# Kernel tuning notes

Measured on AMD Instinct MI355X. Metric: run time of the kernel, lower is better.

Reference implementation:

```python
import jax, jax.numpy as jnp
import numpy as np

N = 100000   # num nodes
D = 128      # node_emb_dim
R = 8        # num_relations
E = 1600000  # num edges


def setup_inputs() -> dict:
    key = jax.random.key(0)
    k0, k1, k2, k3, k4 = jax.random.split(key, 5)
    x = jax.random.normal(k0, (N, D), dtype=jnp.float32)
    edge_index = jax.random.randint(k1, (2, E), 0, N, dtype=jnp.int32)
    edge_type = jax.random.randint(k2, (E,), 0, R, dtype=jnp.int32)
    scale = 1.0 / np.sqrt(D)
    W = (jax.random.normal(k3, (R, D, D), dtype=jnp.float32) * scale)       # per-relation weight
    W_root = (jax.random.normal(k4, (D, D), dtype=jnp.float32) * scale)     # root (self-loop) weight
    bias = jnp.zeros((D,), dtype=jnp.float32)
    return {"x": x, "W": W, "W_root": W_root, "bias": bias,
            "edge_index": edge_index, "edge_type": edge_type}


def reference(x, W, W_root, bias, edge_index, edge_type):
    # PyG RGCNConv (num_bases=None, aggr='mean', root_weight=True, bias=True):
    # out_i = x_i @ W_root + bias + sum_r mean_{j in N_r(i)} x_j @ W_r
    # Mean aggregation is linear, so aggregate neighbor features per (node, relation)
    # first, then apply the per-relation transform (avoids [E,D,D] intermediates).
    src, dst = edge_index[0], edge_index[1]
    seg = dst * R + edge_type                                   # [E] segment id per (dst, rel)
    cnt = jax.ops.segment_sum(jnp.ones((E,), x.dtype), seg, num_segments=N * R)  # [N*R]
    sums = jax.ops.segment_sum(x[src], seg, num_segments=N * R)                   # [N*R, D]
    mean = sums / jnp.maximum(cnt, 1.0)[:, None]                                  # [N*R, D]
    rel_out = jnp.einsum('nrd,rde->ne', mean.reshape(N, R, D), W)                 # [N, D]
    return rel_out + x @ W_root + bias
```

## Files before the change

kernel.cpp:

```cpp
#include <hip/hip_runtime.h>


constexpr int D = 128;
constexpr int R = 8;
constexpr int LDA = 40;
constexpr int TILE2 = 4096;
constexpr int CAP = 3072;
constexpr int MAXRUNS = 8192;
constexpr int TCH = 32;

typedef __bf16 bf16x8 __attribute__((ext_vector_type(8)));
typedef float  f32x4  __attribute__((ext_vector_type(4)));
typedef unsigned short u16x8 __attribute__((ext_vector_type(8)));
typedef unsigned short u16x4 __attribute__((ext_vector_type(4)));

__device__ __forceinline__ unsigned short f2bf(float f) {
    unsigned u = __builtin_bit_cast(unsigned, f);
    u += 0x7FFFu + ((u >> 16) & 1u);
    return (unsigned short)(u >> 16);
}
__device__ __forceinline__ float bf2f(unsigned short h) {
    return __builtin_bit_cast(float, (unsigned)h << 16);
}

constexpr int XB = 640;
constexpr int WB = 64;
__global__ __launch_bounds__(256)
void prep_kernel(const float* __restrict__ x, unsigned short* __restrict__ xbf,
                 int nquad,
                 const int* __restrict__ dst, const int* __restrict__ et,
                 unsigned short* __restrict__ counts, int E, int nruns, int ntiles,
                 const float* __restrict__ Wroot, const float* __restrict__ W,
                 unsigned short* __restrict__ WallTc) {
    __shared__ int lh[MAXRUNS];
    if (blockIdx.x < XB) {
        int stride = XB * 256;
        for (int i = blockIdx.x * 256 + threadIdx.x; i < nquad; i += stride) {
            float4 v = ((const float4*)x)[i];
            u16x4 o;
            o[0] = f2bf(v.x); o[1] = f2bf(v.y); o[2] = f2bf(v.z); o[3] = f2bf(v.w);
            ((u16x4*)xbf)[i] = o;
        }
    } else if (blockIdx.x < XB + (unsigned)ntiles) {
        int tile = blockIdx.x - XB;
        for (int i = threadIdx.x; i < nruns; i += 256) lh[i] = 0;
        __syncthreads();
        int t0 = tile * TILE2;
        #pragma unroll 4
        for (int j = 0; j < TILE2 / 256; ++j) {
            int e = t0 + j * 256 + threadIdx.x;
            if (e < E) {
                int seg = dst[e] * R + et[e];
                atomicAdd(&lh[seg >> 7], 1);
            }
        }
        __syncthreads();
        unsigned short* row = counts + (size_t)tile * nruns;
        for (int i = threadIdx.x; i < nruns; i += 256) row[i] = (unsigned short)lh[i];
    } else {
        int b = blockIdx.x - XB - ntiles;
        int stride = WB * 256;
        for (int idx = b * 256 + threadIdx.x; idx < 128 * 1152; idx += stride) {
            int n = idx / 1152, k = idx % 1152;
            float v = (k < 1024)
                ? W[(size_t)(k >> 7) * 16384 + (size_t)(k & 127) * 128 + n]
                : Wroot[(size_t)(k - 1024) * 128 + n];
            WallTc[idx] = f2bf(v);
        }
    }
}

__global__ __launch_bounds__(256)
void colscanA_kernel(const unsigned short* __restrict__ counts, int* __restrict__ part,
                     int ntiles, int nruns, int cpt) {
    int r = blockIdx.x * 256 + threadIdx.x;
    int c = blockIdx.y;
    if (r >= nruns) return;
    int t0 = c * cpt, t1 = min(t0 + cpt, ntiles);
    int acc = 0;
    for (int t = t0; t < t1; ++t) acc += counts[(size_t)t * nruns + r];
    part[(size_t)c * nruns + r] = acc;
}

__global__ __launch_bounds__(256)
void colscanB_kernel(int* __restrict__ part, int* __restrict__ runtot,
                     int nchunks, int nruns) {
    int r = blockIdx.x * 256 + threadIdx.x;
    if (r >= nruns) return;
    int acc = 0;
    for (int c = 0; c < nchunks; ++c) {
        size_t i = (size_t)c * nruns + r;
        int v = part[i];
        part[i] = acc;
        acc += v;
    }
    runtot[r] = acc;
}

__global__ __launch_bounds__(256)
void colscanC_kernel(unsigned short* __restrict__ counts, const int* __restrict__ part,
                     int ntiles, int nruns, int cpt) {
    int r = blockIdx.x * 256 + threadIdx.x;
    int c = blockIdx.y;
    if (r >= nruns) return;
    int t0 = c * cpt, t1 = min(t0 + cpt, ntiles);
    int acc = part[(size_t)c * nruns + r];
    for (int t = t0; t < t1; ++t) {
        size_t i = (size_t)t * nruns + r;
        int v = counts[i];
        counts[i] = (unsigned short)acc;
        acc += v;
    }
}

__global__ __launch_bounds__(64)
void runscan_kernel(const int* __restrict__ runtot, int* __restrict__ runbase, int nb) {
    int lane = threadIdx.x;
    int carry = 0;
    for (int base = 0; base < nb; base += 64) {
        int i = base + lane;
        int orig = (i < nb) ? runtot[i] : 0;
        int v = orig;
        #pragma unroll
        for (int off = 1; off < 64; off <<= 1) {
            int u = __shfl_up(v, off, 64);
            if (lane >= off) v += u;
        }
        int tot = __shfl(v, 63, 64);
        if (i < nb) runbase[i] = carry + (v - orig);
        carry += tot;
    }
    if (lane == 0) runbase[nb] = carry;
}

__global__ __launch_bounds__(256)
void place_kernel(const int* __restrict__ src, const int* __restrict__ dst,
                  const int* __restrict__ et, const unsigned short* __restrict__ counts,
                  const int* __restrict__ runbase, unsigned* __restrict__ epack,
                  int E, int nruns) {
    __shared__ int lh[MAXRUNS];
    for (int i = threadIdx.x; i < nruns; i += 256) lh[i] = 0;
    __syncthreads();
    int t0 = blockIdx.x * TILE2;
    const unsigned short* colpre = counts + (size_t)blockIdx.x * nruns;
    #pragma unroll 4
    for (int j = 0; j < TILE2 / 256; ++j) {
        int e = t0 + j * 256 + threadIdx.x;
        if (e < E) {
            int seg  = dst[e] * R + et[e];
            int run  = seg >> 7;
            int rank = atomicAdd(&lh[run], 1);
            int pos  = runbase[run] + (int)colpre[run] + rank;
            epack[pos] = (unsigned)src[e] | ((unsigned)(seg & 127) << 24);
        }
    }
}

__global__ __launch_bounds__(256)
void aggregate_kernel(const unsigned short* __restrict__ xbf,
                      const unsigned* __restrict__ epack,
                      const int* __restrict__ runbase,
                      unsigned short* __restrict__ mean,
                      int nseg, int c0) {
    __shared__ unsigned raw[CAP];
    __shared__ unsigned srt[CAP];
    __shared__ int hist[128], sc[128], offs[128], cur[128];

    const int tid  = threadIdx.x;
    const int run  = blockIdx.x;
    const int base = runbase[run];
    const int size = runbase[run + 1] - base;
    const int c8   = tid & 7;
    const int sg0  = tid >> 3;

    float a[4][8] = {};
    int   cacc[4] = {};

    const int nchunks = (size + CAP - 1) / CAP;
    for (int ch = 0; ch < nchunks; ++ch) {
        int off = ch * CAP;
        int n   = min(CAP, size - off);

        if (tid < 128) hist[tid] = 0;
        __syncthreads();
        for (int j = tid; j < n; j += 256) {
            unsigned e = epack[base + off + j];
            raw[j] = e;
            atomicAdd(&hist[e >> 24], 1);
        }
        __syncthreads();
        if (tid < 128) sc[tid] = hist[tid];
        __syncthreads();
        for (int o = 1; o < 128; o <<= 1) {
            int u = 0;
            if (tid < 128 && tid >= o) u = sc[tid - o];
            __syncthreads();
            if (tid < 128) sc[tid] += u;
            __syncthreads();
        }
        if (tid < 128) { int x0 = sc[tid] - hist[tid]; offs[tid] = x0; cur[tid] = x0; }
        __syncthreads();
        for (int j = tid; j < n; j += 256) {
            unsigned e = raw[j];
            int r = atomicAdd(&cur[e >> 24], 1);
            srt[r] = e;
        }
        __syncthreads();
        #pragma unroll
        for (int i = 0; i < 4; ++i) {
            int s  = sg0 + i * 32;
            int st = offs[s], cn = hist[s];
            cacc[i] += cn;
            for (int k = 0; k < cn; k += 4) {
                unsigned e0 = srt[st + k];
                int s1ok = (k + 1 < cn), s2ok = (k + 2 < cn), s3ok = (k + 3 < cn);
                unsigned e1 = s1ok ? srt[st + k + 1] : 0;
                unsigned e2 = s2ok ? srt[st + k + 2] : 0;
                unsigned e3 = s3ok ? srt[st + k + 3] : 0;
                u16x8 v0 = *(const u16x8*)(xbf + ((size_t)(e0 & 0xFFFFFF) << 7) + c0 + c8 * 8);
                #pragma unroll
                for (int q = 0; q < 8; ++q) a[i][q] += bf2f(v0[q]);
                if (s1ok) {
                    u16x8 v = *(const u16x8*)(xbf + ((size_t)(e1 & 0xFFFFFF) << 7) + c0 + c8 * 8);
                    #pragma unroll
                    for (int q = 0; q < 8; ++q) a[i][q] += bf2f(v[q]);
                }
                if (s2ok) {
                    u16x8 v = *(const u16x8*)(xbf + ((size_t)(e2 & 0xFFFFFF) << 7) + c0 + c8 * 8);
                    #pragma unroll
                    for (int q = 0; q < 8; ++q) a[i][q] += bf2f(v[q]);
                }
                if (s3ok) {
                    u16x8 v = *(const u16x8*)(xbf + ((size_t)(e3 & 0xFFFFFF) << 7) + c0 + c8 * 8);
                    #pragma unroll
                    for (int q = 0; q < 8; ++q) a[i][q] += bf2f(v[q]);
                }
            }
        }
        __syncthreads();
    }

    #pragma unroll
    for (int i = 0; i < 4; ++i) {
        int seg = run * 128 + sg0 + i * 32;
        if (seg < nseg) {
            float inv = (cacc[i] > 0) ? 1.0f / (float)cacc[i] : 0.0f;
            u16x8 o;
            #pragma unroll
            for (int q = 0; q < 8; ++q) o[q] = f2bf(a[i][q] * inv);
            *(u16x8*)(mean + ((size_t)seg << 6) + c8 * 8) = o;
        }
    }
}

__global__ __launch_bounds__(256)
void mfma_gemm_kernel(const unsigned short* __restrict__ xbf,
                      const unsigned short* __restrict__ mean0,
                      const unsigned short* __restrict__ mean1,
                      const unsigned short* __restrict__ WallTc,
                      const float* __restrict__ bias,
                      float* __restrict__ out, int N) {
    constexpr int NT = 36;
    __shared__ unsigned short As[2][64 * LDA];
    __shared__ unsigned short Bs[2][128 * LDA];
    const int tid  = threadIdx.x;
    const int nd0  = blockIdx.x * 64;
    const int lane = tid & 63;
    const int wid  = tid >> 6;
    const int wm   = wid >> 1;
    const int wn   = wid & 1;
    const int arow = tid >> 2;
    const int aoct = tid & 3;
    const int brow = tid >> 1;
    const int bhalf = tid & 1;

    f32x4 acc[2][4] = {};

    const int  anode = nd0 + arow;
    const bool aok   = anode < N;

    auto loadG = [&](int kt, u16x8& av8, u16x8& b0, u16x8& b1) {
        #pragma unroll
        for (int j = 0; j < 8; ++j) av8[j] = 0;
        int kbase;
        if (kt < 4) {
            if (aok)
                av8 = *(const u16x8*)(xbf + ((size_t)anode << 7) + kt * 32 + aoct * 8);
            kbase = 1024 + kt * 32;
        } else {
            int lk = (kt - 4) * 32;
            int r  = lk >> 7;
            int c  = lk & 127;
            const unsigned short* mbuf = (c & 64) ? mean1 : mean0;
            if (aok)
                av8 = *(const u16x8*)(mbuf + (((size_t)anode * 8 + r) << 6)
                                      + (c & 63) + aoct * 8);
            kbase = lk;
        }
        const u16x8* wp = (const u16x8*)(WallTc + (size_t)brow * 1152 + kbase + bhalf * 16);
        b0 = wp[0];
        b1 = wp[1];
    };

    u16x8 av8, b0, b1;
    loadG(0, av8, b0, b1);
    *(u16x8*)&As[0][arow * LDA + aoct * 8]       = av8;
    *(u16x8*)&Bs[0][brow * LDA + bhalf * 16]     = b0;
    *(u16x8*)&Bs[0][brow * LDA + bhalf * 16 + 8] = b1;
    __syncthreads();

    const int ko = (lane >> 4) * 8;
    const int rl = lane & 15;

    for (int kt = 0; kt < NT; ++kt) {
        const int cb = kt & 1;
        if (kt + 1 < NT) loadG(kt + 1, av8, b0, b1);

        bf16x8 af[2], bf[4];
        #pragma unroll
        for (int f = 0; f < 2; ++f)
            af[f] = __builtin_bit_cast(bf16x8,
                *(const u16x8*)&As[cb][(wm * 32 + f * 16 + rl) * LDA + ko]);
        #pragma unroll
        for (int f = 0; f < 4; ++f)
            bf[f] = __builtin_bit_cast(bf16x8,
                *(const u16x8*)&Bs[cb][(wn * 64 + f * 16 + rl) * LDA + ko]);
        #pragma unroll
        for (int mf = 0; mf < 2; ++mf)
            #pragma unroll
            for (int nf = 0; nf < 4; ++nf)
                acc[mf][nf] = __builtin_amdgcn_mfma_f32_16x16x32_bf16(af[mf], bf[nf],
                                                                     acc[mf][nf], 0, 0, 0);
        if (kt + 1 < NT) {
            const int nb = cb ^ 1;
            *(u16x8*)&As[nb][arow * LDA + aoct * 8]       = av8;
            *(u16x8*)&Bs[nb][brow * LDA + bhalf * 16]     = b0;
            *(u16x8*)&Bs[nb][brow * LDA + bhalf * 16 + 8] = b1;
            __syncthreads();
        }
    }

    const int rg = lane >> 4;
    #pragma unroll
    for (int nf = 0; nf < 4; ++nf) {
        int n = wn * 64 + nf * 16 + rl;
        float bb = bias[n];
        #pragma unroll
        for (int mf = 0; mf < 2; ++mf) {
            #pragma unroll
            for (int i = 0; i < 4; ++i) {
                int nd = nd0 + wm * 32 + mf * 16 + rg * 4 + i;
                if (nd < N) out[(size_t)nd * 128 + n] = acc[mf][nf][i] + bb;
            }
        }
    }
}

extern "C" void kernel_launch(void* const* d_in, const int* in_sizes, int n_in,
                              void* d_out, int out_size, void* d_ws, size_t ws_size,
                              hipStream_t stream) {
    const float* x     = (const float*)d_in[0];
    const float* W     = (const float*)d_in[1];
    const float* Wroot = (const float*)d_in[2];
    const float* bias  = (const float*)d_in[3];
    const int*   ei    = (const int*)d_in[4];
    const int*   et    = (const int*)d_in[5];
    float*       out   = (float*)d_out;

    const int N = in_sizes[0] / D;
    const int E = in_sizes[5];
    const int* src = ei;
    const int* dst = ei + E;

    const int NSEG   = N * R;
    const int NRUNS  = (NSEG + 127) / 128;
    const int NTILES = (E + TILE2 - 1) / TILE2;
    if (NRUNS > MAXRUNS) return;

    const size_t mean_half    = (size_t)NSEG * 64 * 2;
    const size_t xbf_bytes    = (size_t)N * D * 2;
    const size_t walltc_bytes = (size_t)128 * 1152 * 2;
    const size_t counts_bytes = (size_t)NTILES * NRUNS * 2;
    const size_t part_bytes   = (size_t)TCH * NRUNS * 4;
    const size_t need = 2 * mean_half + xbf_bytes + walltc_bytes + counts_bytes +
                        part_bytes + ((size_t)NRUNS + (NRUNS + 1) + E) * 4 + 512;
    if (ws_size < need) return;

    char* p = (char*)d_ws;
    unsigned short* mean0  = (unsigned short*)p;  p += mean_half;
    unsigned short* mean1  = (unsigned short*)p;  p += mean_half;
    unsigned short* xbf    = (unsigned short*)p;  p += xbf_bytes;
    unsigned short* WallTc = (unsigned short*)p;  p += walltc_bytes;
    unsigned short* counts = (unsigned short*)p;  p += counts_bytes;
    int*      part    = (int*)p;       p += part_bytes;
    int*      runtot  = (int*)p;       p += (size_t)NRUNS * 4;
    int*      runbase = (int*)p;       p += (size_t)(NRUNS + 1) * 4;
    unsigned* epack   = (unsigned*)p;

    prep_kernel<<<XB + NTILES + WB, 256, 0, stream>>>(
        x, xbf, N * D / 4, dst, et, counts, E, NRUNS, NTILES, Wroot, W, WallTc);

    const int cpt = (NTILES + TCH - 1) / TCH;
    dim3 cgrid((NRUNS + 255) / 256, TCH);
    colscanA_kernel<<<cgrid, 256, 0, stream>>>(counts, part, NTILES, NRUNS, cpt);
    colscanB_kernel<<<(NRUNS + 255) / 256, 256, 0, stream>>>(part, runtot, TCH, NRUNS);
    colscanC_kernel<<<cgrid, 256, 0, stream>>>(counts, part, NTILES, NRUNS, cpt);
    runscan_kernel<<<1, 64, 0, stream>>>(runtot, runbase, NRUNS);

    place_kernel<<<NTILES, 256, 0, stream>>>(src, dst, et, counts, runbase, epack, E, NRUNS);

    aggregate_kernel<<<NRUNS, 256, 0, stream>>>(xbf, epack, runbase, mean0, NSEG, 0);
    aggregate_kernel<<<NRUNS, 256, 0, stream>>>(xbf, epack, runbase, mean1, NSEG, 64);

    const int gx = (N + 63) / 64;
    mfma_gemm_kernel<<<gx, 256, 0, stream>>>(xbf, mean0, mean1, WallTc, bias, out, N);
}
```

Measured before the change: 358.3 us.

## Fuse aggregation halves into one pass and triple-buffer GEMM tiles

Measured after the change: 351.4 us. Within noise of the previous version (-1.9%).

```diff
diff --git a/kernel.cpp b/kernel.cpp
--- a/kernel.cpp
+++ b/kernel.cpp
@@ -161,7 +161,7 @@
                       const unsigned* __restrict__ epack,
                       const int* __restrict__ runbase,
                       unsigned short* __restrict__ mean,
-                      int nseg, int c0) {
+                      int nseg) {
     __shared__ unsigned raw[CAP];
     __shared__ unsigned srt[CAP];
     __shared__ int hist[128], sc[128], offs[128], cur[128];
@@ -170,11 +170,11 @@
     const int run  = blockIdx.x;
     const int base = runbase[run];
     const int size = runbase[run + 1] - base;
-    const int c8   = tid & 7;
-    const int sg0  = tid >> 3;
-
-    float a[4][8] = {};
-    int   cacc[4] = {};
+    const int c8   = tid & 15;
+    const int sg0  = tid >> 4;
+
+    float a[8][8] = {};
+    int   cacc[8] = {};
 
     const int nchunks = (size + CAP - 1) / CAP;
     for (int ch = 0; ch < nchunks; ++ch) {
@@ -207,8 +207,8 @@
         }
         __syncthreads();
         #pragma unroll
-        for (int i = 0; i < 4; ++i) {
-            int s  = sg0 + i * 32;
+        for (int i = 0; i < 8; ++i) {
+            int s  = sg0 + i * 16;
             int st = offs[s], cn = hist[s];
             cacc[i] += cn;
             for (int k = 0; k < cn; k += 4) {
@@ -217,21 +217,21 @@
                 unsigned e1 = s1ok ? srt[st + k + 1] : 0;
                 unsigned e2 = s2ok ? srt[st + k + 2] : 0;
                 unsigned e3 = s3ok ? srt[st + k + 3] : 0;
-                u16x8 v0 = *(const u16x8*)(xbf + ((size_t)(e0 & 0xFFFFFF) << 7) + c0 + c8 * 8);
+                u16x8 v0 = *(const u16x8*)(xbf + ((size_t)(e0 & 0xFFFFFF) << 7) + c8 * 8);
                 #pragma unroll
                 for (int q = 0; q < 8; ++q) a[i][q] += bf2f(v0[q]);
                 if (s1ok) {
-                    u16x8 v = *(const u16x8*)(xbf + ((size_t)(e1 & 0xFFFFFF) << 7) + c0 + c8 * 8);
+                    u16x8 v = *(const u16x8*)(xbf + ((size_t)(e1 & 0xFFFFFF) << 7) + c8 * 8);
                     #pragma unroll
                     for (int q = 0; q < 8; ++q) a[i][q] += bf2f(v[q]);
                 }
                 if (s2ok) {
-                    u16x8 v = *(const u16x8*)(xbf + ((size_t)(e2 & 0xFFFFFF) << 7) + c0 + c8 * 8);
+                    u16x8 v = *(const u16x8*)(xbf + ((size_t)(e2 & 0xFFFFFF) << 7) + c8 * 8);
                     #pragma unroll
                     for (int q = 0; q < 8; ++q) a[i][q] += bf2f(v[q]);
                 }
                 if (s3ok) {
-                    u16x8 v = *(const u16x8*)(xbf + ((size_t)(e3 & 0xFFFFFF) << 7) + c0 + c8 * 8);
+                    u16x8 v = *(const u16x8*)(xbf + ((size_t)(e3 & 0xFFFFFF) << 7) + c8 * 8);
                     #pragma unroll
                     for (int q = 0; q < 8; ++q) a[i][q] += bf2f(v[q]);
                 }
@@ -241,28 +241,30 @@
     }
 
     #pragma unroll
-    for (int i = 0; i < 4; ++i) {
-        int seg = run * 128 + sg0 + i * 32;
+    for (int i = 0; i < 8; ++i) {
+        int seg = run * 128 + sg0 + i * 16;
         if (seg < nseg) {
+            int node = seg >> 3, r = seg & 7;
             float inv = (cacc[i] > 0) ? 1.0f / (float)cacc[i] : 0.0f;
             u16x8 o;
             #pragma unroll
             for (int q = 0; q < 8; ++q) o[q] = f2bf(a[i][q] * inv);
-            *(u16x8*)(mean + ((size_t)seg << 6) + c8 * 8) = o;
+            *(u16x8*)(mean + ((size_t)node << 10) + r * 128 + c8 * 8) = o;
         }
     }
 }
 
 __global__ __launch_bounds__(256)
 void mfma_gemm_kernel(const unsigned short* __restrict__ xbf,
-                      const unsigned short* __restrict__ mean0,
-                      const unsigned short* __restrict__ mean1,
+                      const unsigned short* __restrict__ mean,
                       const unsigned short* __restrict__ WallTc,
                       const float* __restrict__ bias,
                       float* __restrict__ out, int N) {
     constexpr int NT = 36;
-    __shared__ unsigned short As[2][64 * LDA];
-    __shared__ unsigned short Bs[2][128 * LDA];
+    constexpr int ABUF = 64 * LDA;
+    constexpr int BBUF = 128 * LDA;
+    __shared__ unsigned short As[3][ABUF];
+    __shared__ unsigned short Bs[3][BBUF];
     const int tid  = threadIdx.x;
     const int nd0  = blockIdx.x * 64;
     const int lane = tid & 63;
@@ -289,54 +291,59 @@
             kbase = 1024 + kt * 32;
         } else {
             int lk = (kt - 4) * 32;
-            int r  = lk >> 7;
-            int c  = lk & 127;
-            const unsigned short* mbuf = (c & 64) ? mean1 : mean0;
             if (aok)
-                av8 = *(const u16x8*)(mbuf + (((size_t)anode * 8 + r) << 6)
-                                      + (c & 63) + aoct * 8);
+                av8 = *(const u16x8*)(mean + ((size_t)anode << 10) + lk + aoct * 8);
             kbase = lk;
         }
         const u16x8* wp = (const u16x8*)(WallTc + (size_t)brow * 1152 + kbase + bhalf * 16);
         b0 = wp[0];
         b1 = wp[1];
     };
-
-    u16x8 av8, b0, b1;
-    loadG(0, av8, b0, b1);
-    *(u16x8*)&As[0][arow * LDA + aoct * 8]       = av8;
-    *(u16x8*)&Bs[0][brow * LDA + bhalf * 16]     = b0;
-    *(u16x8*)&Bs[0][brow * LDA + bhalf * 16 + 8] = b1;
-    __syncthreads();
+    auto storeT = [&](int buf, const u16x8& av8, const u16x8& b0, const u16x8& b1) {
+        *(u16x8*)&As[buf][arow * LDA + aoct * 8]       = av8;
+        *(u16x8*)&Bs[buf][brow * LDA + bhalf * 16]     = b0;
+        *(u16x8*)&Bs[buf][brow * LDA + bhalf * 16 + 8] = b1;
+    };
 
     const int ko = (lane >> 4) * 8;
     const int rl = lane & 15;
-
-    for (int kt = 0; kt < NT; ++kt) {
-        const int cb = kt & 1;
-        if (kt + 1 < NT) loadG(kt + 1, av8, b0, b1);
-
+    auto compute = [&](int buf) {
         bf16x8 af[2], bf[4];
         #pragma unroll
         for (int f = 0; f < 2; ++f)
             af[f] = __builtin_bit_cast(bf16x8,
-                *(const u16x8*)&As[cb][(wm * 32 + f * 16 + rl) * LDA + ko]);
+                *(const u16x8*)&As[buf][(wm * 32 + f * 16 + rl) * LDA + ko]);
         #pragma unroll
         for (int f = 0; f < 4; ++f)
             bf[f] = __builtin_bit_cast(bf16x8,
-                *(const u16x8*)&Bs[cb][(wn * 64 + f * 16 + rl) * LDA + ko]);
+                *(const u16x8*)&Bs[buf][(wn * 64 + f * 16 + rl) * LDA + ko]);
         #pragma unroll
         for (int mf = 0; mf < 2; ++mf)
             #pragma unroll
             for (int nf = 0; nf < 4; ++nf)
                 acc[mf][nf] = __builtin_amdgcn_mfma_f32_16x16x32_bf16(af[mf], bf[nf],
                                                                      acc[mf][nf], 0, 0, 0);
+    };
+
+    u16x8 aA, bA0, bA1, aB, bB0, bB1;
+    loadG(0, aA, bA0, bA1);
+    storeT(0, aA, bA0, bA1);
+    loadG(1, aA, bA0, bA1);
+    __syncthreads();
+
+    int cb = 0;
+    for (int kt = 0; kt < NT; kt += 2) {
+        if (kt + 2 < NT) loadG(kt + 2, aB, bB0, bB1);
+        compute(cb);
+        if (kt + 1 < NT) storeT((cb + 1) % 3, aA, bA0, bA1);
+        __syncthreads();
+        cb = (cb + 1) % 3;
         if (kt + 1 < NT) {
-            const int nb = cb ^ 1;
-            *(u16x8*)&As[nb][arow * LDA + aoct * 8]       = av8;
-            *(u16x8*)&Bs[nb][brow * LDA + bhalf * 16]     = b0;
-            *(u16x8*)&Bs[nb][brow * LDA + bhalf * 16 + 8] = b1;
+            if (kt + 3 < NT) loadG(kt + 3, aA, bA0, bA1);
+            compute(cb);
+            if (kt + 2 < NT) storeT((cb + 1) % 3, aB, bB0, bB1);
             __syncthreads();
+            cb = (cb + 1) % 3;
         }
     }
 
@@ -377,18 +384,17 @@
     const int NTILES = (E + TILE2 - 1) / TILE2;
     if (NRUNS > MAXRUNS) return;
 
-    const size_t mean_half    = (size_t)NSEG * 64 * 2;
+    const size_t mean_bytes   = (size_t)N * 1024 * 2;
     const size_t xbf_bytes    = (size_t)N * D * 2;
     const size_t walltc_bytes = (size_t)128 * 1152 * 2;
     const size_t counts_bytes = (size_t)NTILES * NRUNS * 2;
     const size_t part_bytes   = (size_t)TCH * NRUNS * 4;
-    const size_t need = 2 * mean_half + xbf_bytes + walltc_bytes + counts_bytes +
+    const size_t need = mean_bytes + xbf_bytes + walltc_bytes + counts_bytes +
                         part_bytes + ((size_t)NRUNS + (NRUNS + 1) + E) * 4 + 512;
     if (ws_size < need) return;
 
     char* p = (char*)d_ws;
-    unsigned short* mean0  = (unsigned short*)p;  p += mean_half;
-    unsigned short* mean1  = (unsigned short*)p;  p += mean_half;
+    unsigned short* mean   = (unsigned short*)p;  p += mean_bytes;
     unsigned short* xbf    = (unsigned short*)p;  p += xbf_bytes;
     unsigned short* WallTc = (unsigned short*)p;  p += walltc_bytes;
     unsigned short* counts = (unsigned short*)p;  p += counts_bytes;
@@ -409,9 +415,8 @@
 
     place_kernel<<<NTILES, 256, 0, stream>>>(src, dst, et, counts, runbase, epack, E, NRUNS);
 
-    aggregate_kernel<<<NRUNS, 256, 0, stream>>>(xbf, epack, runbase, mean0, NSEG, 0);
-    aggregate_kernel<<<NRUNS, 256, 0, stream>>>(xbf, epack, runbase, mean1, NSEG, 64);
+    aggregate_kernel<<<NRUNS, 256, 0, stream>>>(xbf, epack, runbase, mean, NSEG);
 
     const int gx = (N + 63) / 64;
-    mfma_gemm_kernel<<<gx, 256, 0, stream>>>(xbf, mean0, mean1, WallTc, bias, out, N);
-}
+    mfma_gemm_kernel<<<gx, 256, 0, stream>>>(xbf, mean, WallTc, bias, out, N);
+}
```
